# Performance work log

Hardware: AMD Instinct MI355X
Metric: run time of the kernel (lower is better)

## Reference

```python
import jax, jax.numpy as jnp
import numpy as np

SQRT2 = 1.4142135623730951
B, C, T, J = 32, 4, 262144, 8


def _dw_corr(x, f):
    # depthwise VALID cross-correlation of (B,C,T) with 1-D filter f
    ch = x.shape[1]
    w = jnp.tile(f[None, None, :], (ch, 1, 1))  # (C,1,m)
    return jax.lax.conv_general_dilated(
        x, w, (1,), 'VALID', feature_group_count=ch,
        dimension_numbers=('NCH', 'OIH', 'NCH'))


def colfilter(x, h):
    # 'same' true convolution with odd-length filter h, zero padding
    p = h.shape[0] // 2
    xp = jnp.pad(x, ((0, 0), (0, 0), (p, p)))
    return _dw_corr(xp, jnp.flip(h))


def colifilt(x, ha, hb):
    # dtcwt synthesis upsampling filter bank (even-length qshift filters,
    # m//2 odd for 10-tap), zero extension (padding_mode='zeros').
    # Output length 2T; phase convention of dtcwt colifilt with ta=t, tb=t-1.
    b, c, t = x.shape
    m2 = ha.shape[0] // 2  # 5 for 10-tap qshift
    xp = jnp.pad(x, ((0, 0), (0, 0), (m2, m2)))  # length t+10
    L = t // 2 + 4
    seq_b = xp[:, :, 1::2][:, :, :L]      # padded indices 1,3,...,t+7
    seq_a = xp[:, :, 0::2][:, :, 1:L + 1]  # padded indices 2,4,...,t+8
    hao, hae = jnp.flip(ha[0::2]), jnp.flip(ha[1::2])  # odd/even taps of tree-a filter
    hbo, hbe = jnp.flip(hb[0::2]), jnp.flip(hb[1::2])
    y0 = _dw_corr(seq_b, hao)  # output samples 4s
    y1 = _dw_corr(seq_a, hbo)  # 4s+1
    y2 = _dw_corr(seq_b, hae)  # 4s+2
    y3 = _dw_corr(seq_a, hbe)  # 4s+3
    return jnp.stack([y0, y1, y2, y3], axis=-1).reshape(b, c, 2 * t)


def c2q(bp_r, bp_i, scale):
    # complex -> real: real part to even samples, imag part to odd samples
    b, c, th = bp_r.shape
    return (jnp.stack([bp_r, bp_i], axis=-1) * scale).reshape(b, c, 2 * th)


def inv_j2plus(lo, bp_r, bp_i, g0a, g1a, g0b, g1b):
    # one coarse synthesis level: interleave complex bandpass, then
    hi = c2q(bp_r, bp_i, SQRT2)
    return colifilt(lo, g0b, g0a) + colifilt(hi, g1b, g1a)


def inv_j1(lo, bp_r, bp_i, g0o, g1o):
    # finest synthesis level: full-rate biorthogonal filters, no upsampling
    hi = c2q(bp_r, bp_i, SQRT2)
    return colfilter(lo, g0o) + colfilter(hi, g1o)


def setup_inputs():
    key = jax.random.key(0)
    ks = jax.random.split(key, 32)
    inp = {}
    inp['yl'] = jax.random.normal(ks[0], (B, C, T // 2 ** (J - 1)), jnp.float32)
    for j in range(J):
        tj = T // 2 ** (j + 1)
        inp[f'yh{j}_r'] = jax.random.normal(ks[2 * j + 1], (B, C, tj), jnp.float32)
        inp[f'yh{j}_i'] = jax.random.normal(ks[2 * j + 2], (B, C, tj), jnp.float32)

    def filt(k, n):
        f = jax.random.normal(k, (n,), jnp.float32)
        return f / jnp.linalg.norm(f)

    inp['g0o'] = filt(ks[20], 7)   # near_sym_a synthesis lowpass (7-tap)
    inp['g1o'] = filt(ks[21], 5)   # near_sym_a synthesis highpass (5-tap)
    g0a = filt(ks[22], 10)         # qshift_a 10-tap
    g1a = filt(ks[23], 10)
    inp['g0a'], inp['g0b'] = g0a, jnp.flip(g0a)  # tree-b = time-reversed tree-a
    inp['g1a'], inp['g1b'] = g1a, jnp.flip(g1a)
    return inp


def reference(yl, yh0_r, yh0_i, yh1_r, yh1_i, yh2_r, yh2_i, yh3_r, yh3_i,
              yh4_r, yh4_i, yh5_r, yh5_i, yh6_r, yh6_i, yh7_r, yh7_i,
              g0o, g1o, g0a, g0b, g1a, g1b):
    yh = [(yh0_r, yh0_i), (yh1_r, yh1_i), (yh2_r, yh2_i), (yh3_r, yh3_i),
          (yh4_r, yh4_i), (yh5_r, yh5_i), (yh6_r, yh6_i), (yh7_r, yh7_i)]
    x = yl
    for j in range(J - 1, 0, -1):  # coarse-to-fine, doubles length each level
        x = inv_j2plus(x, yh[j][0], yh[j][1], g0a, g1a, g0b, g1b)
    return inv_j1(x, yh[0][0], yh[0][1], g0o, g1o)
```

## Files before the change

### kernel.cpp

```cpp
#include <hip/hip_runtime.h>

#define PBLOCK 256
#define FBLOCK 128
#define FT 1024

typedef float v2f __attribute__((ext_vector_type(2)));

static __device__ __forceinline__ float ldz(const float* __restrict__ p, int i, int n) {
    return (i >= 0 && i < n) ? p[i] : 0.f;
}

#define BAR_LGKM() do { \
    asm volatile("s_waitcnt lgkmcnt(0)" ::: "memory"); \
    __builtin_amdgcn_s_barrier(); \
} while (0)

#define BAR_FULL() do { \
    asm volatile("s_waitcnt vmcnt(0) lgkmcnt(0)" ::: "memory"); \
    __builtin_amdgcn_s_barrier(); \
} while (0)

#define AS1C(p) ((const __attribute__((address_space(1))) unsigned int*)(p))
#define AS3(p)  ((__attribute__((address_space(3))) unsigned int*)(p))

struct QFilt {
    float b0e[5], b0o[5], a0e[5], a0o[5];
    float b1e[5], b1o[5], a1e[5], a1o[5];
};

static __device__ __forceinline__ QFilt load_qfilt(
    const float* __restrict__ g0a, const float* __restrict__ g0b,
    const float* __restrict__ g1a, const float* __restrict__ g1b) {
    const float S2 = 1.4142135623730951f;
    QFilt f;
#pragma unroll
    for (int i = 0; i < 5; ++i) {
        f.b0e[i] = g0b[8 - 2 * i]; f.b0o[i] = g0b[9 - 2 * i];
        f.a0e[i] = g0a[8 - 2 * i]; f.a0o[i] = g0a[9 - 2 * i];
        f.b1e[i] = S2 * g1b[8 - 2 * i]; f.b1o[i] = S2 * g1b[9 - 2 * i];
        f.a1e[i] = S2 * g1a[8 - 2 * i]; f.a1o[i] = S2 * g1a[9 - 2 * i];
    }
    return f;
}

struct QFiltP {
    v2f f01l[5], f23l[5], f01h[5], f23h[5];
};

static __device__ __forceinline__ QFiltP load_qfiltp(
    const float* __restrict__ g0a, const float* __restrict__ g0b,
    const float* __restrict__ g1a, const float* __restrict__ g1b) {
    const float S2 = 1.4142135623730951f;
    QFiltP f;
#pragma unroll
    for (int i = 0; i < 5; ++i) {
        float b0e = g0b[8 - 2 * i], b0o = g0b[9 - 2 * i];
        float a0e = g0a[8 - 2 * i], a0o = g0a[9 - 2 * i];
        float b1e = S2 * g1b[8 - 2 * i], b1o = S2 * g1b[9 - 2 * i];
        float a1e = S2 * g1a[8 - 2 * i], a1o = S2 * g1a[9 - 2 * i];
        f.f01l[i] = (v2f){b0e, a0e};
        f.f23l[i] = (v2f){b0o, a0o};
        f.f01h[i] = (v2f){b1e, a1e};
        f.f23h[i] = (v2f){b1o, a1o};
    }
    return f;
}

static __device__ __forceinline__ float4 quad_p(
    const float* base, int loOff, int riOff, int ioff, const QFiltP& f) {
    v2f y01 = (v2f){0.f, 0.f}, y23 = (v2f){0.f, 0.f};
#pragma unroll
    for (int i = 0; i < 5; ++i) {
        v2f lo2 = *reinterpret_cast<const v2f*>(base + loOff + 2 * i);
        v2f ri;
        ri.x = base[riOff + i];
        ri.y = base[riOff + ioff + i];
        y01 = __builtin_elementwise_fma(lo2, f.f01l[i], y01);
        y23 = __builtin_elementwise_fma(lo2, f.f23l[i], y23);
        y01 = __builtin_elementwise_fma(ri, f.f01h[i], y01);
        y23 = __builtin_elementwise_fma(ri, f.f23h[i], y23);
    }
    return make_float4(y01.x, y01.y, y23.x, y23.y);
}

static __device__ __forceinline__ float4 quad_i(
    const float* __restrict__ lo_s, int lobase,
    const float* __restrict__ r_s, const float* __restrict__ i_s, int ribase,
    const QFilt& f) {
    float y0 = 0.f, y1 = 0.f, y2 = 0.f, y3 = 0.f;
#pragma unroll
    for (int i = 0; i < 5; ++i) {
        float ve = lo_s[lobase + 2 * i], vo = lo_s[lobase + 2 * i + 1];
        float vr = r_s[ribase + i], vi = i_s[ribase + i];
        y0 = fmaf(ve, f.b0e[i], y0); y2 = fmaf(ve, f.b0o[i], y2);
        y1 = fmaf(vo, f.a0e[i], y1); y3 = fmaf(vo, f.a0o[i], y3);
        y0 = fmaf(vr, f.b1e[i], y0); y2 = fmaf(vr, f.b1o[i], y2);
        y1 = fmaf(vi, f.a1e[i], y1); y3 = fmaf(vi, f.a1o[i], y3);
    }
    return make_float4(y0, y1, y2, y3);
}

static __device__ __forceinline__ float4 quad_d(
    const float* __restrict__ Ae, const float* __restrict__ Ao, int base,
    const float* __restrict__ r_s, const float* __restrict__ i_s, int ribase,
    const QFilt& f) {
    float y0 = 0.f, y1 = 0.f, y2 = 0.f, y3 = 0.f;
#pragma unroll
    for (int i = 0; i < 5; ++i) {
        float ve = Ae[base + i], vo = Ao[base + i];
        float vr = r_s[ribase + i], vi = i_s[ribase + i];
        y0 = fmaf(ve, f.b0e[i], y0); y2 = fmaf(ve, f.b0o[i], y2);
        y1 = fmaf(vo, f.a0e[i], y1); y3 = fmaf(vo, f.a0o[i], y3);
        y0 = fmaf(vr, f.b1e[i], y0); y2 = fmaf(vr, f.b1o[i], y2);
        y1 = fmaf(vi, f.a1e[i], y1); y3 = fmaf(vi, f.a1o[i], y3);
    }
    return make_float4(y0, y1, y2, y3);
}

__global__ void __launch_bounds__(PBLOCK) pair_lvl(
    const float* __restrict__ up,
    const float* __restrict__ ru, const float* __restrict__ iu,
    const float* __restrict__ rl, const float* __restrict__ il,
    float* __restrict__ out,
    const float* __restrict__ g0a, const float* __restrict__ g0b,
    const float* __restrict__ g1a, const float* __restrict__ g1b,
    int L)
{
    __shared__ __align__(16) float upw[272], ruw[140], iuw[140], rlw[264], ilw[264];
    __shared__ __align__(16) float Ae[260], Ao[260];
    int tid = threadIdx.x, bx = blockIdx.x, row = blockIdx.y;
    int lup = L >> 2, lu8 = L >> 3, lql = L >> 2;
    const float* uprow = up + (size_t)row * lup;
    const float* rurow = ru + (size_t)row * lu8;
    const float* iurow = iu + (size_t)row * lu8;
    const float* rlrow = rl + (size_t)row * lql;
    const float* ilrow = il + (size_t)row * lql;
    bool bnd = (bx == 0) || (bx == (int)gridDim.x - 1);
    int S = bx << 8;
    int sAu = (S >> 1) - 1;
    int gu = S - 8;
    int gru = (S >> 1) - 4;
    int grl = S - 4;

    for (int i = tid; i < 270; i += PBLOCK) {
        const float* src; float* dst; int k, gb, len;
        if (i < 68)       { src = uprow; dst = upw; k = i;       gb = gu + 4 * k;  len = lup; }
        else if (i < 103) { src = rurow; dst = ruw; k = i - 68;  gb = gru + 4 * k; len = lu8; }
        else if (i < 138) { src = iurow; dst = iuw; k = i - 103; gb = gru + 4 * k; len = lu8; }
        else if (i < 204) { src = rlrow; dst = rlw; k = i - 138; gb = grl + 4 * k; len = lql; }
        else              { src = ilrow; dst = ilw; k = i - 204; gb = grl + 4 * k; len = lql; }
        float4 v;
        if (!bnd) v = *reinterpret_cast<const float4*>(src + gb);
        else { v.x = ldz(src, gb, len); v.y = ldz(src, gb + 1, len);
               v.z = ldz(src, gb + 2, len); v.w = ldz(src, gb + 3, len); }
        *reinterpret_cast<float4*>(dst + 4 * k) = v;
    }
    __syncthreads();

    QFilt f = load_qfilt(g0a, g0b, g1a, g1b);
    if (tid < 130) {
        float4 q = quad_i(upw, 2 * tid + 2, ruw, iuw, tid + 1, f);
        if (bnd) {
            int sp = sAu + tid;
            if (sp < 0 || sp >= lu8) q = make_float4(0.f, 0.f, 0.f, 0.f);
        }
        Ae[2 * tid] = q.x; Ae[2 * tid + 1] = q.z;
        Ao[2 * tid] = q.y; Ao[2 * tid + 1] = q.w;
    }
    __syncthreads();

    float4 res = quad_d(Ae, Ao, tid, rlw, ilw, tid + 2, f);
    reinterpret_cast<float4*>(out + (size_t)row * L)[S + tid] = res;
}

#define O_X4 0
#define O_R3 148
#define O_I3 224
#define O_R2 300
#define O_I2 440
#define O_R1 580
#define O_I1 844
#define O_X3 1108
#define O_X2 1388
#define O_X1 1916
#define W_TOT 2948
#define NSLOT 277

static __device__ __forceinline__ void slot_map(
    int i, int v0, int u0, int s0, int t4, int t8, int t16,
    const float* x4row, const float* r3row, const float* i3row,
    const float* r2row, const float* i2row,
    const float* r1row, const float* i1row,
    const float*& src, int& gb, int& len)
{
    if (i < 37)       { src = x4row; int k = i;       gb = 2 * v0 - 8 + 4 * k; len = t8;  }
    else if (i < 56)  { src = r3row; int k = i - 37;  gb = v0 - 4 + 4 * k;     len = t16; }
    else if (i < 75)  { src = i3row; int k = i - 56;  gb = v0 - 4 + 4 * k;     len = t16; }
    else if (i < 110) { src = r2row; int k = i - 75;  gb = u0 - 4 + 4 * k;     len = t8;  }
    else if (i < 145) { src = i2row; int k = i - 110; gb = u0 - 4 + 4 * k;     len = t8;  }
    else if (i < 211) { src = r1row; int k = i - 145; gb = s0 - 4 + 4 * k;     len = t4;  }
    else              { src = i1row; int k = i - 211; gb = s0 - 4 + 4 * k;     len = t4;  }
}

__global__ void __launch_bounds__(FBLOCK) final4_async(
    const float* __restrict__ x4,
    const float* __restrict__ r3, const float* __restrict__ i3,
    const float* __restrict__ r2, const float* __restrict__ i2,
    const float* __restrict__ r1, const float* __restrict__ i1,
    const float* __restrict__ r0, const float* __restrict__ i0,
    float* __restrict__ out,
    const float* __restrict__ g0a, const float* __restrict__ g0b,
    const float* __restrict__ g1a, const float* __restrict__ g1b,
    const float* __restrict__ g0o, const float* __restrict__ g1o,
    int T_)
{
    const float S2 = 1.4142135623730951f;
    __shared__ __align__(16) float W[W_TOT];

    int row = blockIdx.y, tid = threadIdx.x, bx = blockIdx.x;
    int t2 = T_ >> 1, t4 = T_ >> 2, t8 = T_ >> 3, t16 = T_ >> 4;
    int s0 = bx << 8, u0 = bx << 7, v0 = bx << 6, h0 = bx << 9;
    const float* x4row = x4 + (size_t)row * t8;
    const float* r3row = r3 + (size_t)row * t16;
    const float* i3row = i3 + (size_t)row * t16;
    const float* r2row = r2 + (size_t)row * t8;
    const float* i2row = i2 + (size_t)row * t8;
    const float* r1row = r1 + (size_t)row * t4;
    const float* i1row = i1 + (size_t)row * t4;
    const float* r0row = r0 + (size_t)row * t2;
    const float* i0row = i0 + (size_t)row * t2;
    bool bnd = (bx == 0) || (bx == (int)gridDim.x - 1);

    if (!bnd) {
#pragma unroll
        for (int it = 0; it < 2; ++it) {
            int i = tid + FBLOCK * it;
            const float* src; int gb, len;
            slot_map(i, v0, u0, s0, t4, t8, t16,
                     x4row, r3row, i3row, r2row, i2row, r1row, i1row, src, gb, len);
            __builtin_amdgcn_global_load_lds(AS1C(src + gb), AS3(W + 4 * i), 16, 0, 0);
        }
        if (tid < NSLOT - 2 * FBLOCK) {
            int i = tid + 2 * FBLOCK;
            const float* src; int gb, len;
            slot_map(i, v0, u0, s0, t4, t8, t16,
                     x4row, r3row, i3row, r2row, i2row, r1row, i1row, src, gb, len);
            __builtin_amdgcn_global_load_lds(AS1C(src + gb), AS3(W + 4 * i), 16, 0, 0);
        }
    } else {
#pragma unroll
        for (int it = 0; it < 3; ++it) {
            int i = tid + FBLOCK * it;
            if (i < NSLOT) {
                const float* src; int gb, len;
                slot_map(i, v0, u0, s0, t4, t8, t16,
                         x4row, r3row, i3row, r2row, i2row, r1row, i1row, src, gb, len);
                float4 v;
                v.x = ldz(src, gb, len);     v.y = ldz(src, gb + 1, len);
                v.z = ldz(src, gb + 2, len); v.w = ldz(src, gb + 3, len);
                *reinterpret_cast<float4*>(W + 4 * i) = v;
            }
        }
    }
    BAR_FULL();

    float rA[6], iA[6];
    {
        int u0e = h0 + 4 * tid - 1;
        if (!bnd) {
            float4 va = *reinterpret_cast<const float4*>(r0row + u0e);
            float2 va2 = *reinterpret_cast<const float2*>(r0row + u0e + 4);
            float4 vb = *reinterpret_cast<const float4*>(i0row + u0e);
            float2 vb2 = *reinterpret_cast<const float2*>(i0row + u0e + 4);
            rA[0] = va.x; rA[1] = va.y; rA[2] = va.z; rA[3] = va.w;
            rA[4] = va2.x; rA[5] = va2.y;
            iA[0] = vb.x; iA[1] = vb.y; iA[2] = vb.z; iA[3] = vb.w;
            iA[4] = vb2.x; iA[5] = vb2.y;
        } else {
#pragma unroll
            for (int e = 0; e < 6; ++e) {
                rA[e] = ldz(r0row, u0e + e, t2);
                iA[e] = ldz(i0row, u0e + e, t2);
            }
        }
    }

    QFiltP f = load_qfiltp(g0a, g0b, g1a, g1b);
    float g0r[7], g1r[5];
#pragma unroll
    for (int j = 0; j < 7; ++j) g0r[j] = g0o[j];
#pragma unroll
    for (int j = 0; j < 5; ++j) g1r[j] = S2 * g1o[j];

    if (tid < 69) {
        int k = tid;
        float4 q = quad_p(W, O_X4 + 2 * k, O_R3 + k, 76, f);
        if (bnd) {
            int v = v0 - 2 + k;
            if (v < 0 || v >= t16) q = make_float4(0.f, 0.f, 0.f, 0.f);
        }
        *reinterpret_cast<float4*>(W + O_X3 + 4 * k) = q;
    }
    BAR_LGKM();

    {
        int k = tid;
        float4 q = quad_p(W, O_X3 + 2 * k, O_R2 + k, 140, f);
        if (bnd) {
            int u = u0 - 2 + k;
            if (u < 0 || u >= t8) q = make_float4(0.f, 0.f, 0.f, 0.f);
        }
        *reinterpret_cast<float4*>(W + O_X2 + 4 * k) = q;
        if (tid < 4) {
            int k2 = tid + FBLOCK;
            q = quad_p(W, O_X3 + 2 * k2, O_R2 + k2, 140, f);
            if (bnd) {
                int u = u0 - 2 + k2;
                if (u < 0 || u >= t8) q = make_float4(0.f, 0.f, 0.f, 0.f);
            }
            *reinterpret_cast<float4*>(W + O_X2 + 4 * k2) = q;
        }
    }
    BAR_LGKM();

    float4 mq0, mq1;
    {
        int l = 2 * tid;
        mq0 = quad_p(W, O_X2 + 2 * l + 2, O_R1 + l + 1, 264, f);
        mq1 = quad_p(W, O_X2 + 2 * l + 4, O_R1 + l + 2, 264, f);
        if (bnd) {
            int s = s0 - 1 + l;
            if (s < 0 || s >= t4)         mq0 = make_float4(0.f, 0.f, 0.f, 0.f);
            if (s + 1 < 0 || s + 1 >= t4) mq1 = make_float4(0.f, 0.f, 0.f, 0.f);
        }
        *reinterpret_cast<float4*>(W + O_X1 + 4 * l) = mq0;
        *reinterpret_cast<float4*>(W + O_X1 + 4 * (l + 1)) = mq1;
        if (tid < 2) {
            int l2 = 256 + tid;
            float4 q = quad_p(W, O_X2 + 2 * l2 + 2, O_R1 + l2 + 1, 264, f);
            if (bnd) {
                int s = s0 - 1 + l2;
                if (s < 0 || s >= t4) q = make_float4(0.f, 0.f, 0.f, 0.f);
            }
            *reinterpret_cast<float4*>(W + O_X1 + 4 * l2) = q;
        }
    }
    BAR_LGKM();

    float w[16];
    *reinterpret_cast<float4*>(&w[0])  = mq0;
    *reinterpret_cast<float4*>(&w[4])  = mq1;
    *reinterpret_cast<float4*>(&w[8])  = *reinterpret_cast<const float4*>(W + O_X1 + 4 * (2 * tid + 2));
    *reinterpret_cast<float4*>(&w[12]) = *reinterpret_cast<const float4*>(W + O_X1 + 4 * (2 * tid + 3));

    float o[8];
#pragma unroll
    for (int p = 0; p < 8; ++p) {
        float acc = 0.f;
#pragma unroll
        for (int j = 0; j < 7; ++j)
            acc = fmaf(g0r[j], w[p + 7 - j], acc);
#pragma unroll
        for (int j = 0; j < 5; ++j) {
            int e = p + 4 - j;
            float v = (e & 1) ? iA[e >> 1] : rA[e >> 1];
            acc = fmaf(g1r[j], v, acc);
        }
        o[p] = acc;
    }
    float4* op = reinterpret_cast<float4*>(out + (size_t)row * T_) + s0 + 2 * tid;
    op[0] = make_float4(o[0], o[1], o[2], o[3]);
    op[1] = make_float4(o[4], o[5], o[6], o[7]);
}

extern "C" void kernel_launch(void* const* d_in, const int* in_sizes, int n_in,
                              void* d_out, int out_size, void* d_ws, size_t ws_size,
                              hipStream_t stream)
{
    const float* yl = (const float*)d_in[0];
    const float* yhr[8]; const float* yhi[8];
    for (int j = 0; j < 8; ++j) {
        yhr[j] = (const float*)d_in[1 + 2 * j];
        yhi[j] = (const float*)d_in[2 + 2 * j];
    }
    const float* g0o = (const float*)d_in[17];
    const float* g1o = (const float*)d_in[18];
    const float* g0a = (const float*)d_in[19];
    const float* g0b = (const float*)d_in[20];
    const float* g1a = (const float*)d_in[21];
    const float* g1b = (const float*)d_in[22];

    const int BC = 32 * 4;
    const int T_ = 262144;

    float* x4buf = (float*)d_ws;
    float* x6buf = (float*)((char*)d_ws + ((size_t)32 << 20));

    {
        dim3 grid(8192 / 1024, BC);
        pair_lvl<<<grid, PBLOCK, 0, stream>>>(
            yl, yhr[7], yhi[7], yhr[6], yhi[6], x6buf,
            g0a, g0b, g1a, g1b, 8192);
    }
    {
        dim3 grid(32768 / 1024, BC);
        pair_lvl<<<grid, PBLOCK, 0, stream>>>(
            x6buf, yhr[5], yhi[5], yhr[4], yhi[4], x4buf,
            g0a, g0b, g1a, g1b, 32768);
    }
    dim3 grid(T_ / FT, BC);
    final4_async<<<grid, FBLOCK, 0, stream>>>(
        x4buf, yhr[3], yhi[3], yhr[2], yhi[2], yhr[1], yhi[1],
        yhr[0], yhi[0], (float*)d_out,
        g0a, g0b, g1a, g1b, g0o, g1o, T_);
}
```

Measured before the change: 106.3 us.

## Process two tiles per block with double-buffered async LDS staging

```diff
diff --git a/kernel.cpp b/kernel.cpp
--- a/kernel.cpp
+++ b/kernel.cpp
@@ -2,7 +2,6 @@
 
 #define PBLOCK 256
 #define FBLOCK 128
-#define FT 1024
 
 typedef float v2f __attribute__((ext_vector_type(2)));
 
@@ -180,10 +179,11 @@
 #define O_I2 440
 #define O_R1 580
 #define O_I1 844
-#define O_X3 1108
-#define O_X2 1388
-#define O_X1 1916
-#define W_TOT 2948
+#define SBUF 1108
+#define O_X3 2216
+#define O_X2 2496
+#define O_X1 3024
+#define W_TOT 4056
 #define NSLOT 277
 
 static __device__ __forceinline__ void slot_map(
@@ -202,7 +202,143 @@
     else              { src = i1row; int k = i - 211; gb = s0 - 4 + 4 * k;     len = t4;  }
 }
 
-__global__ void __launch_bounds__(FBLOCK) final4_async(
+static __device__ __forceinline__ void stage_async_tile(
+    float* W, int sb, int gtile, int wv, int lane,
+    int t4, int t8, int t16,
+    const float* x4row, const float* r3row, const float* i3row,
+    const float* r2row, const float* i2row,
+    const float* r1row, const float* i1row)
+{
+    int v0 = gtile << 6, u0 = gtile << 7, s0 = gtile << 8;
+    int base_w = wv ? 139 : 0;
+    int lim_w  = wv ? 277 : 139;
+#pragma unroll
+    for (int s = 0; s < 3; ++s) {
+        int slot = base_w + 64 * s + lane;
+        if (slot < lim_w) {
+            const float* src; int gb, len;
+            slot_map(slot, v0, u0, s0, t4, t8, t16,
+                     x4row, r3row, i3row, r2row, i2row, r1row, i1row, src, gb, len);
+            __builtin_amdgcn_global_load_lds(AS1C(src + gb), AS3(W + sb + 4 * slot), 16, 0, 0);
+        }
+    }
+}
+
+static __device__ __forceinline__ void stage_reg_tile(
+    float* W, int sb, int gtile, int tid,
+    int t4, int t8, int t16,
+    const float* x4row, const float* r3row, const float* i3row,
+    const float* r2row, const float* i2row,
+    const float* r1row, const float* i1row)
+{
+    int v0 = gtile << 6, u0 = gtile << 7, s0 = gtile << 8;
+#pragma unroll
+    for (int it = 0; it < 3; ++it) {
+        int i = tid + FBLOCK * it;
+        if (i < NSLOT) {
+            const float* src; int gb, len;
+            slot_map(i, v0, u0, s0, t4, t8, t16,
+                     x4row, r3row, i3row, r2row, i2row, r1row, i1row, src, gb, len);
+            float4 v;
+            v.x = ldz(src, gb, len);     v.y = ldz(src, gb + 1, len);
+            v.z = ldz(src, gb + 2, len); v.w = ldz(src, gb + 3, len);
+            *reinterpret_cast<float4*>(W + sb + 4 * i) = v;
+        }
+    }
+}
+
+template<bool BND>
+static __device__ __forceinline__ void tile_phases(
+    float* W, int SB, int gtile, int tid,
+    int t4, int t8, int t16, int T_,
+    const QFiltP& f, const float* g0r, const float* g1r,
+    const float rA[6], const float iA[6],
+    float* __restrict__ outrow)
+{
+    int s0 = gtile << 8, u0 = gtile << 7, v0 = gtile << 6;
+
+    if (tid < 69) {
+        int k = tid;
+        float4 q = quad_p(W, SB + O_X4 + 2 * k, SB + O_R3 + k, 76, f);
+        if (BND) {
+            int v = v0 - 2 + k;
+            if (v < 0 || v >= t16) q = make_float4(0.f, 0.f, 0.f, 0.f);
+        }
+        *reinterpret_cast<float4*>(W + O_X3 + 4 * k) = q;
+    }
+    BAR_LGKM();
+
+    {
+        int k = tid;
+        float4 q = quad_p(W, O_X3 + 2 * k, SB + O_R2 + k, 140, f);
+        if (BND) {
+            int u = u0 - 2 + k;
+            if (u < 0 || u >= t8) q = make_float4(0.f, 0.f, 0.f, 0.f);
+        }
+        *reinterpret_cast<float4*>(W + O_X2 + 4 * k) = q;
+        if (tid < 4) {
+            int k2 = tid + FBLOCK;
+            q = quad_p(W, O_X3 + 2 * k2, SB + O_R2 + k2, 140, f);
+            if (BND) {
+                int u = u0 - 2 + k2;
+                if (u < 0 || u >= t8) q = make_float4(0.f, 0.f, 0.f, 0.f);
+            }
+            *reinterpret_cast<float4*>(W + O_X2 + 4 * k2) = q;
+        }
+    }
+    BAR_LGKM();
+
+    float4 mq0, mq1;
+    {
+        int l = 2 * tid;
+        mq0 = quad_p(W, O_X2 + 2 * l + 2, SB + O_R1 + l + 1, 264, f);
+        mq1 = quad_p(W, O_X2 + 2 * l + 4, SB + O_R1 + l + 2, 264, f);
+        if (BND) {
+            int s = s0 - 1 + l;
+            if (s < 0 || s >= t4)         mq0 = make_float4(0.f, 0.f, 0.f, 0.f);
+            if (s + 1 < 0 || s + 1 >= t4) mq1 = make_float4(0.f, 0.f, 0.f, 0.f);
+        }
+        *reinterpret_cast<float4*>(W + O_X1 + 4 * l) = mq0;
+        *reinterpret_cast<float4*>(W + O_X1 + 4 * (l + 1)) = mq1;
+        if (tid < 2) {
+            int l2 = 256 + tid;
+            float4 q = quad_p(W, O_X2 + 2 * l2 + 2, SB + O_R1 + l2 + 1, 264, f);
+            if (BND) {
+                int s = s0 - 1 + l2;
+                if (s < 0 || s >= t4) q = make_float4(0.f, 0.f, 0.f, 0.f);
+            }
+            *reinterpret_cast<float4*>(W + O_X1 + 4 * l2) = q;
+        }
+    }
+    BAR_LGKM();
+
+    float w[16];
+    *reinterpret_cast<float4*>(&w[0])  = mq0;
+    *reinterpret_cast<float4*>(&w[4])  = mq1;
+    *reinterpret_cast<float4*>(&w[8])  = *reinterpret_cast<const float4*>(W + O_X1 + 4 * (2 * tid + 2));
+    *reinterpret_cast<float4*>(&w[12]) = *reinterpret_cast<const float4*>(W + O_X1 + 4 * (2 * tid + 3));
+
+    float o[8];
+#pragma unroll
+    for (int p = 0; p < 8; ++p) {
+        float acc = 0.f;
+#pragma unroll
+        for (int j = 0; j < 7; ++j)
+            acc = fmaf(g0r[j], w[p + 7 - j], acc);
+#pragma unroll
+        for (int j = 0; j < 5; ++j) {
+            int e = p + 4 - j;
+            float v = (e & 1) ? iA[e >> 1] : rA[e >> 1];
+            acc = fmaf(g1r[j], v, acc);
+        }
+        o[p] = acc;
+    }
+    float4* op = reinterpret_cast<float4*>(outrow) + s0 + 2 * tid;
+    op[0] = make_float4(o[0], o[1], o[2], o[3]);
+    op[1] = make_float4(o[4], o[5], o[6], o[7]);
+}
+
+__global__ void __launch_bounds__(FBLOCK) final4_dt(
     const float* __restrict__ x4,
     const float* __restrict__ r3, const float* __restrict__ i3,
     const float* __restrict__ r2, const float* __restrict__ i2,
@@ -218,8 +354,9 @@
     __shared__ __align__(16) float W[W_TOT];
 
     int row = blockIdx.y, tid = threadIdx.x, bx = blockIdx.x;
+    int lane = tid & 63, wv = tid >> 6;
     int t2 = T_ >> 1, t4 = T_ >> 2, t8 = T_ >> 3, t16 = T_ >> 4;
-    int s0 = bx << 8, u0 = bx << 7, v0 = bx << 6, h0 = bx << 9;
+    int g0t = 2 * bx, g1t = 2 * bx + 1;
     const float* x4row = x4 + (size_t)row * t8;
     const float* r3row = r3 + (size_t)row * t16;
     const float* i3row = i3 + (size_t)row * t16;
@@ -229,148 +366,97 @@
     const float* i1row = i1 + (size_t)row * t4;
     const float* r0row = r0 + (size_t)row * t2;
     const float* i0row = i0 + (size_t)row * t2;
+    float* outrow = out + (size_t)row * T_;
     bool bnd = (bx == 0) || (bx == (int)gridDim.x - 1);
 
+    float rA0[6], iA0[6], rA1[6], iA1[6];
+    float g0r[7], g1r[5];
+
     if (!bnd) {
-#pragma unroll
-        for (int it = 0; it < 2; ++it) {
-            int i = tid + FBLOCK * it;
-            const float* src; int gb, len;
-            slot_map(i, v0, u0, s0, t4, t8, t16,
-                     x4row, r3row, i3row, r2row, i2row, r1row, i1row, src, gb, len);
-            __builtin_amdgcn_global_load_lds(AS1C(src + gb), AS3(W + 4 * i), 16, 0, 0);
-        }
-        if (tid < NSLOT - 2 * FBLOCK) {
-            int i = tid + 2 * FBLOCK;
-            const float* src; int gb, len;
-            slot_map(i, v0, u0, s0, t4, t8, t16,
-                     x4row, r3row, i3row, r2row, i2row, r1row, i1row, src, gb, len);
-            __builtin_amdgcn_global_load_lds(AS1C(src + gb), AS3(W + 4 * i), 16, 0, 0);
-        }
-    } else {
-#pragma unroll
-        for (int it = 0; it < 3; ++it) {
-            int i = tid + FBLOCK * it;
-            if (i < NSLOT) {
-                const float* src; int gb, len;
-                slot_map(i, v0, u0, s0, t4, t8, t16,
-                         x4row, r3row, i3row, r2row, i2row, r1row, i1row, src, gb, len);
-                float4 v;
-                v.x = ldz(src, gb, len);     v.y = ldz(src, gb + 1, len);
-                v.z = ldz(src, gb + 2, len); v.w = ldz(src, gb + 3, len);
-                *reinterpret_cast<float4*>(W + 4 * i) = v;
-            }
-        }
-    }
-    BAR_FULL();
-
-    float rA[6], iA[6];
-    {
-        int u0e = h0 + 4 * tid - 1;
-        if (!bnd) {
+        stage_async_tile(W, 0, g0t, wv, lane, t4, t8, t16,
+                         x4row, r3row, i3row, r2row, i2row, r1row, i1row);
+        __builtin_amdgcn_sched_barrier(0);
+        {
+            int u0e = (g0t << 9) + 4 * tid - 1;
             float4 va = *reinterpret_cast<const float4*>(r0row + u0e);
             float2 va2 = *reinterpret_cast<const float2*>(r0row + u0e + 4);
             float4 vb = *reinterpret_cast<const float4*>(i0row + u0e);
             float2 vb2 = *reinterpret_cast<const float2*>(i0row + u0e + 4);
-            rA[0] = va.x; rA[1] = va.y; rA[2] = va.z; rA[3] = va.w;
-            rA[4] = va2.x; rA[5] = va2.y;
-            iA[0] = vb.x; iA[1] = vb.y; iA[2] = vb.z; iA[3] = vb.w;
-            iA[4] = vb2.x; iA[5] = vb2.y;
-        } else {
+            rA0[0] = va.x; rA0[1] = va.y; rA0[2] = va.z; rA0[3] = va.w;
+            rA0[4] = va2.x; rA0[5] = va2.y;
+            iA0[0] = vb.x; iA0[1] = vb.y; iA0[2] = vb.z; iA0[3] = vb.w;
+            iA0[4] = vb2.x; iA0[5] = vb2.y;
+        }
+        __builtin_amdgcn_sched_barrier(0);
+        stage_async_tile(W, SBUF, g1t, wv, lane, t4, t8, t16,
+                         x4row, r3row, i3row, r2row, i2row, r1row, i1row);
+        __builtin_amdgcn_sched_barrier(0);
+        {
+            int u0e = (g1t << 9) + 4 * tid - 1;
+            float4 va = *reinterpret_cast<const float4*>(r0row + u0e);
+            float2 va2 = *reinterpret_cast<const float2*>(r0row + u0e + 4);
+            float4 vb = *reinterpret_cast<const float4*>(i0row + u0e);
+            float2 vb2 = *reinterpret_cast<const float2*>(i0row + u0e + 4);
+            rA1[0] = va.x; rA1[1] = va.y; rA1[2] = va.z; rA1[3] = va.w;
+            rA1[4] = va2.x; rA1[5] = va2.y;
+            iA1[0] = vb.x; iA1[1] = vb.y; iA1[2] = vb.z; iA1[3] = vb.w;
+            iA1[4] = vb2.x; iA1[5] = vb2.y;
+        }
+        __builtin_amdgcn_sched_barrier(0);
+
+        QFiltP f = load_qfiltp(g0a, g0b, g1a, g1b);
+#pragma unroll
+        for (int j = 0; j < 7; ++j) g0r[j] = g0o[j];
+#pragma unroll
+        for (int j = 0; j < 5; ++j) g1r[j] = S2 * g1o[j];
+
+        asm volatile("s_waitcnt vmcnt(11) lgkmcnt(0)" ::: "memory");
+        __builtin_amdgcn_s_barrier();
+
+        tile_phases<false>(W, 0, g0t, tid, t4, t8, t16, T_, f, g0r, g1r,
+                           rA0, iA0, outrow);
+
+        asm volatile("s_waitcnt vmcnt(6) lgkmcnt(0)" ::: "memory");
+        __builtin_amdgcn_s_barrier();
+
+        tile_phases<false>(W, SBUF, g1t, tid, t4, t8, t16, T_, f, g0r, g1r,
+                           rA1, iA1, outrow);
+    } else {
+        QFiltP f = load_qfiltp(g0a, g0b, g1a, g1b);
+#pragma unroll
+        for (int j = 0; j < 7; ++j) g0r[j] = g0o[j];
+#pragma unroll
+        for (int j = 0; j < 5; ++j) g1r[j] = S2 * g1o[j];
+
+        stage_reg_tile(W, 0, g0t, tid, t4, t8, t16,
+                       x4row, r3row, i3row, r2row, i2row, r1row, i1row);
+        {
+            int u0e = (g0t << 9) + 4 * tid - 1;
 #pragma unroll
             for (int e = 0; e < 6; ++e) {
-                rA[e] = ldz(r0row, u0e + e, t2);
-                iA[e] = ldz(i0row, u0e + e, t2);
+                rA0[e] = ldz(r0row, u0e + e, t2);
+                iA0[e] = ldz(i0row, u0e + e, t2);
             }
         }
-    }
-
-    QFiltP f = load_qfiltp(g0a, g0b, g1a, g1b);
-    float g0r[7], g1r[5];
-#pragma unroll
-    for (int j = 0; j < 7; ++j) g0r[j] = g0o[j];
-#pragma unroll
-    for (int j = 0; j < 5; ++j) g1r[j] = S2 * g1o[j];
-
-    if (tid < 69) {
-        int k = tid;
-        float4 q = quad_p(W, O_X4 + 2 * k, O_R3 + k, 76, f);
-        if (bnd) {
-            int v = v0 - 2 + k;
-            if (v < 0 || v >= t16) q = make_float4(0.f, 0.f, 0.f, 0.f);
-        }
-        *reinterpret_cast<float4*>(W + O_X3 + 4 * k) = q;
-    }
-    BAR_LGKM();
-
-    {
-        int k = tid;
-        float4 q = quad_p(W, O_X3 + 2 * k, O_R2 + k, 140, f);
-        if (bnd) {
-            int u = u0 - 2 + k;
-            if (u < 0 || u >= t8) q = make_float4(0.f, 0.f, 0.f, 0.f);
-        }
-        *reinterpret_cast<float4*>(W + O_X2 + 4 * k) = q;
-        if (tid < 4) {
-            int k2 = tid + FBLOCK;
-            q = quad_p(W, O_X3 + 2 * k2, O_R2 + k2, 140, f);
-            if (bnd) {
-                int u = u0 - 2 + k2;
-                if (u < 0 || u >= t8) q = make_float4(0.f, 0.f, 0.f, 0.f);
+        BAR_FULL();
+        tile_phases<true>(W, 0, g0t, tid, t4, t8, t16, T_, f, g0r, g1r,
+                          rA0, iA0, outrow);
+        BAR_FULL();
+
+        stage_reg_tile(W, SBUF, g1t, tid, t4, t8, t16,
+                       x4row, r3row, i3row, r2row, i2row, r1row, i1row);
+        {
+            int u0e = (g1t << 9) + 4 * tid - 1;
+#pragma unroll
+            for (int e = 0; e < 6; ++e) {
+                rA1[e] = ldz(r0row, u0e + e, t2);
+                iA1[e] = ldz(i0row, u0e + e, t2);
             }
-            *reinterpret_cast<float4*>(W + O_X2 + 4 * k2) = q;
-        }
-    }
-    BAR_LGKM();
-
-    float4 mq0, mq1;
-    {
-        int l = 2 * tid;
-        mq0 = quad_p(W, O_X2 + 2 * l + 2, O_R1 + l + 1, 264, f);
-        mq1 = quad_p(W, O_X2 + 2 * l + 4, O_R1 + l + 2, 264, f);
-        if (bnd) {
-            int s = s0 - 1 + l;
-            if (s < 0 || s >= t4)         mq0 = make_float4(0.f, 0.f, 0.f, 0.f);
-            if (s + 1 < 0 || s + 1 >= t4) mq1 = make_float4(0.f, 0.f, 0.f, 0.f);
-        }
-        *reinterpret_cast<float4*>(W + O_X1 + 4 * l) = mq0;
-        *reinterpret_cast<float4*>(W + O_X1 + 4 * (l + 1)) = mq1;
-        if (tid < 2) {
-            int l2 = 256 + tid;
-            float4 q = quad_p(W, O_X2 + 2 * l2 + 2, O_R1 + l2 + 1, 264, f);
-            if (bnd) {
-                int s = s0 - 1 + l2;
-                if (s < 0 || s >= t4) q = make_float4(0.f, 0.f, 0.f, 0.f);
-            }
-            *reinterpret_cast<float4*>(W + O_X1 + 4 * l2) = q;
-        }
-    }
-    BAR_LGKM();
-
-    float w[16];
-    *reinterpret_cast<float4*>(&w[0])  = mq0;
-    *reinterpret_cast<float4*>(&w[4])  = mq1;
-    *reinterpret_cast<float4*>(&w[8])  = *reinterpret_cast<const float4*>(W + O_X1 + 4 * (2 * tid + 2));
-    *reinterpret_cast<float4*>(&w[12]) = *reinterpret_cast<const float4*>(W + O_X1 + 4 * (2 * tid + 3));
-
-    float o[8];
-#pragma unroll
-    for (int p = 0; p < 8; ++p) {
-        float acc = 0.f;
-#pragma unroll
-        for (int j = 0; j < 7; ++j)
-            acc = fmaf(g0r[j], w[p + 7 - j], acc);
-#pragma unroll
-        for (int j = 0; j < 5; ++j) {
-            int e = p + 4 - j;
-            float v = (e & 1) ? iA[e >> 1] : rA[e >> 1];
-            acc = fmaf(g1r[j], v, acc);
-        }
-        o[p] = acc;
-    }
-    float4* op = reinterpret_cast<float4*>(out + (size_t)row * T_) + s0 + 2 * tid;
-    op[0] = make_float4(o[0], o[1], o[2], o[3]);
-    op[1] = make_float4(o[4], o[5], o[6], o[7]);
+        }
+        BAR_FULL();
+        tile_phases<true>(W, SBUF, g1t, tid, t4, t8, t16, T_, f, g0r, g1r,
+                          rA1, iA1, outrow);
+    }
 }
 
 extern "C" void kernel_launch(void* const* d_in, const int* in_sizes, int n_in,
@@ -408,8 +494,8 @@
             x6buf, yhr[5], yhi[5], yhr[4], yhi[4], x4buf,
             g0a, g0b, g1a, g1b, 32768);
     }
-    dim3 grid(T_ / FT, BC);
-    final4_async<<<grid, FBLOCK, 0, stream>>>(
+    dim3 grid(T_ / 2048, BC);
+    final4_dt<<<grid, FBLOCK, 0, stream>>>(
         x4buf, yhr[3], yhi[3], yhr[2], yhi[2], yhr[1], yhi[1],
         yhr[0], yhi[0], (float*)d_out,
         g0a, g0b, g1a, g1b, g0o, g1o, T_);
```

Result: slower. 108.8 us (+2.3%).
